# Optimization experiments

Hardware: AMD Instinct MI355X
Metric: run time of the kernel (lower is better)

## Reference

```python
import jax, jax.numpy as jnp
import numpy as np

N_ATOMS = 512
ATOM_SHAPE = (3, 3, 3)
SPARSE_ITERS = 128
FPB = 8  # features_per_band


def unit_norm(x, axis=-1, eps=1e-12):
    n = jnp.linalg.norm(x, axis=axis, keepdims=True)
    return x / jnp.maximum(n, eps)


def best_fit(signal, atoms):
    # signal: [B, bands, time, per] ; atoms: [n_atoms, 3,3,3]
    B, bands, time, per = signal.shape
    sig = signal[:, None]  # [B,1,bands,time,per]
    # pad (0,2) on last three dims
    sig = jnp.pad(sig, ((0, 0), (0, 0), (0, 2), (0, 2), (0, 2)))
    # conv3d correlation: lax conv with NCDHW / OIDHW
    fm = jax.lax.conv_general_dilated(
        sig, atoms[:, None], window_strides=(1, 1, 1), padding='VALID',
        dimension_numbers=('NCDHW', 'OIDHW', 'NCDHW'))  # [B, n_atoms, bands, time, per]
    flat = fm.reshape(B, -1)
    idx = jnp.argmax(flat, axis=-1)
    val = jnp.take_along_axis(flat, idx[:, None], axis=-1)[:, 0]
    # unflatten index -> (atom, b, c, d)
    fshape = fm.shape[1:]
    a_i = idx // (fshape[1] * fshape[2] * fshape[3])
    rem = idx % (fshape[1] * fshape[2] * fshape[3])
    b_i = rem // (fshape[2] * fshape[3])
    rem = rem % (fshape[2] * fshape[3])
    c_i = rem // fshape[3]
    d_i = rem % fshape[3]

    def per_batch(sig_b, a, b, c, dd, v):
        # sig_b: padded [bands+2, time+2, per+2]
        atom = atoms[a] * v  # [3,3,3]
        # Since conv output spatial extent = input extent (valid over padded),
        # max offsets b,c,d <= dims-1 of padded-2, slice always fits fully.
        patch = jax.lax.dynamic_slice(sig_b, (b, c, dd), ATOM_SHAPE)
        return jax.lax.dynamic_update_slice(sig_b, patch - atom, (b, c, dd))

    sig2 = jax.vmap(per_batch)(sig[:, 0], a_i, b_i, c_i, d_i, val)
    return sig2[:, :bands, :time, :per]


def sparse_code(signal, atoms):
    def body(res, _):
        return best_fit(res, atoms), None
    res, _ = jax.lax.scan(body, signal, None, length=SPARSE_ITERS)
    return res


def layer_norm(x, g, b, eps=1e-5):
    m = jnp.mean(x, axis=-1, keepdims=True)
    v = jnp.var(x, axis=-1, keepdims=True)
    return (x - m) / jnp.sqrt(v + eps) * g + b


def batch_norm(x, g, b, eps=1e-5):
    # x: [B, C, T]; training-mode batch stats over (B, T)
    m = jnp.mean(x, axis=(0, 2), keepdims=True)
    v = jnp.var(x, axis=(0, 2), keepdims=True)
    return (x - m) / jnp.sqrt(v + eps) * g[None, :, None] + b[None, :, None]


def conv1d(x, w, b, pad):
    # x: [B,C,T], w: [O,I,K]
    y = jax.lax.conv_general_dilated(x, w, (1,), [(pad, pad)],
                                     dimension_numbers=('NCT', 'OIT', 'NCT'))
    return y + b[None, :, None]


def upsample4(x):
    # nearest, scale 4 along time
    return jnp.repeat(x, 4, axis=-1)


def setup_inputs() -> dict:
    key = jax.random.key(0)
    ks = jax.random.split(key, 24)
    w = 0.05
    x = jax.random.normal(ks[0], (4, 128, 128, 257), dtype=jnp.float32)
    d = jax.random.uniform(ks[1], (N_ATOMS, 27), minval=-1, maxval=1)
    atoms = unit_norm(d, axis=-1).reshape(N_ATOMS, *ATOM_SHAPE)
    inp = {
        'x': x,
        'atoms': atoms,
        'embed_w': jax.random.normal(ks[2], (257, FPB)) * w,
        'embed_b': jnp.zeros((FPB,)),
        # LinearOutputStack(1024, 3, out 1024, LayerNorm): 3 hidden-ish linears
        'ctx_w1': jax.random.normal(ks[3], (1024, 1024)) * w,
        'ctx_b1': jnp.zeros((1024,)),
        'ctx_g1': jnp.ones((1024,)), 'ctx_be1': jnp.zeros((1024,)),
        'ctx_w2': jax.random.normal(ks[4], (1024, 1024)) * w,
        'ctx_b2': jnp.zeros((1024,)),
        'ctx_g2': jnp.ones((1024,)), 'ctx_be2': jnp.zeros((1024,)),
        'ctx_w3': jax.random.normal(ks[5], (1024, 1024)) * w,
        'ctx_b3': jnp.zeros((1024,)),
        # up stack conv weights
        'up_w1': jax.random.normal(ks[6], (512, 1024, 7)) * w,
        'up_b1': jnp.zeros((512,)), 'bn_g1': jnp.ones((512,)), 'bn_b1': jnp.zeros((512,)),
        'up_w2': jax.random.normal(ks[7], (256, 512, 7)) * w,
        'up_b2': jnp.zeros((256,)), 'bn_g2': jnp.ones((256,)), 'bn_b2': jnp.zeros((256,)),
        'up_w3': jax.random.normal(ks[8], (128, 256, 7)) * w,
        'up_b3': jnp.zeros((128,)), 'bn_g3': jnp.ones((128,)), 'bn_b3': jnp.zeros((128,)),
        'up_w4': jax.random.normal(ks[9], (64, 128, 7)) * w,
        'up_b4': jnp.zeros((64,)), 'bn_g4': jnp.ones((64,)), 'bn_b4': jnp.zeros((64,)),
        'up_w5': jax.random.normal(ks[10], (1, 64, 7)) * w,
        'up_b5': jnp.zeros((1,)),
    }
    return inp


def reference(x, atoms, embed_w, embed_b,
              ctx_w1, ctx_b1, ctx_g1, ctx_be1,
              ctx_w2, ctx_b2, ctx_g2, ctx_be2,
              ctx_w3, ctx_b3,
              up_w1, up_b1, bn_g1, bn_b1,
              up_w2, up_b2, bn_g2, bn_b2,
              up_w3, up_b3, bn_g3, bn_b3,
              up_w4, up_b4, bn_g4, bn_b4,
              up_w5, up_b5):
    B, bands, time, per = x.shape
    # embed_features
    e = x @ embed_w + embed_b  # [B, bands, time, 8]
    # sparse coding (no_grad in original; result discarded but computed)
    _res = jax.lax.stop_gradient(sparse_code(e, atoms))
    encoded = jnp.transpose(e, (0, 3, 1, 2)).reshape(B, FPB * bands, time)  # [B,1024,T]
    # context
    ctx = jnp.sum(encoded, axis=-1)  # [B,1024]
    h = layer_norm(jax.nn.leaky_relu(ctx @ ctx_w1 + ctx_b1, 0.2), ctx_g1, ctx_be1)
    h = layer_norm(jax.nn.leaky_relu(h @ ctx_w2 + ctx_b2, 0.2), ctx_g2, ctx_be2)
    ctx_out = h @ ctx_w3 + ctx_b3
    # generate (up stack)
    y = jax.nn.leaky_relu(batch_norm(conv1d(encoded, up_w1, up_b1, 3), bn_g1, bn_b1), 0.2)
    y = upsample4(y)
    y = jax.nn.leaky_relu(batch_norm(conv1d(y, up_w2, up_b2, 3), bn_g2, bn_b2), 0.2)
    y = upsample4(y)
    y = jax.nn.leaky_relu(batch_norm(conv1d(y, up_w3, up_b3, 3), bn_g3, bn_b3), 0.2)
    y = upsample4(y)
    y = jax.nn.leaky_relu(batch_norm(conv1d(y, up_w4, up_b4, 3), bn_g4, bn_b4), 0.2)
    y = upsample4(y)
    y = conv1d(y, up_w5, up_b5, 3)  # [B,1,T*256]
    # reverb approximated as identity mix (ReverbGenerator source unavailable)
    return y, ctx_out
```

## Files before the change

### kernel.cpp

```cpp
#include <hip/hip_runtime.h>
#include <hip/hip_bf16.h>

using sh8   = __attribute__((ext_vector_type(8))) short;
using f32x4 = __attribute__((ext_vector_type(4))) float;

#define DEV __device__ __forceinline__

DEV float leaky(float x) { return x >= 0.f ? x : 0.2f * x; }

DEV unsigned short f2bf(float f) {
  unsigned u = __float_as_uint(f);
  u += 0x7FFF + ((u >> 16) & 1);
  return (unsigned short)(u >> 16);
}
DEV float bf2f(unsigned short b) { return __uint_as_float(((unsigned)b) << 16); }

template<int Cout, int Cin>
DEV void pack7_body(const float* __restrict__ w, unsigned short* __restrict__ wp, int blk) {
  constexpr long plane = (long)(Cin >> 5) * Cout * 32;
  int tid = blk * 256 + threadIdx.x;
  if (tid >= Cout * Cin) return;
  int co = tid / Cin, ci = tid - co * Cin;
  const float* src = w + (long)tid * 7;
  unsigned short* dst = wp + ((long)(ci >> 5) * Cout + co) * 32 + (ci & 31);
  #pragma unroll
  for (int k = 0; k < 7; ++k) dst[k * plane] = f2bf(src[k]);
}
template<int Cout, int Cin>
DEV void packph_body(const float* __restrict__ w, unsigned short* __restrict__ wp, int blk) {
  constexpr long plane = (long)(Cin >> 5) * Cout * 32;
  int tid = blk * 256 + threadIdx.x;
  if (tid >= Cout * Cin) return;
  int co = tid / Cin, ci = tid - co * Cin;
  float wk[7];
  #pragma unroll
  for (int k = 0; k < 7; ++k) wk[k] = w[(long)tid * 7 + k];
  unsigned short* dst = wp + ((long)(ci >> 5) * Cout + co) * 32 + (ci & 31);
  #pragma unroll
  for (int p = 0; p < 4; ++p) {
    #pragma unroll
    for (int d = 0; d < 3; ++d) {
      float s = 0.f;
      #pragma unroll
      for (int k = 0; k < 7; ++k) if (((p + k + 1) >> 2) == d) s += wk[k];
      dst[(p * 3 + d) * plane] = f2bf(s);
    }
  }
}

DEV void gemm_body(int gb, const float* __restrict__ h, const float* __restrict__ w,
                   float* __restrict__ gpart, int sum2) {
  __shared__ float hl[4][128];
  __shared__ float red[8][4][32];
  const int jb = gb & 31, kc = gb >> 5, k0 = kc * 128;
  for (int i = threadIdx.x; i < 512; i += 256) {
    int bb = i >> 7, kk = i & 127;
    float v;
    if (sum2) {
      int base = ((bb << 10) + k0 + kk) << 1;
      v = h[base] + h[base + 1];
    } else {
      v = h[(bb << 10) + k0 + kk];
    }
    hl[bb][kk] = v;
  }
  __syncthreads();
  const int jl = threadIdx.x & 31, kq = threadIdx.x >> 5;
  const int j = jb * 32 + jl;
  float a0 = 0, a1 = 0, a2 = 0, a3 = 0;
  const float* wp = w + (long)(k0 + kq * 16) * 1024 + j;
  #pragma unroll
  for (int k = 0; k < 16; ++k) {
    float wv = wp[(long)k * 1024];
    a0 += hl[0][kq * 16 + k] * wv;
    a1 += hl[1][kq * 16 + k] * wv;
    a2 += hl[2][kq * 16 + k] * wv;
    a3 += hl[3][kq * 16 + k] * wv;
  }
  red[kq][0][jl] = a0; red[kq][1][jl] = a1; red[kq][2][jl] = a2; red[kq][3][jl] = a3;
  __syncthreads();
  if (threadIdx.x < 128) {
    int bb = threadIdx.x >> 5, j2 = threadIdx.x & 31;
    float s = 0;
    #pragma unroll
    for (int q = 0; q < 8; ++q) s += red[q][bb][j2];
    gpart[((long)kc * 4 + bb) * 1024 + jb * 32 + j2] = s;
  }
}

__global__ __launch_bounds__(256)
void embed_pack(const float* __restrict__ x, const float* __restrict__ ew,
                const float* __restrict__ eb, unsigned short* __restrict__ encbf,
                float* __restrict__ part,
                const float* __restrict__ cw1, const float* __restrict__ cw2,
                const float* __restrict__ cw3, const float* __restrict__ cw4,
                unsigned short* __restrict__ wbuf) {
  if (blockIdx.x >= 1024) {
    int blk = blockIdx.x - 1024;
    if (blk < 2048)      pack7_body<512, 1024>(cw1, wbuf, blk);
    else if (blk < 2560) packph_body<256, 512>(cw2, wbuf + 3670016, blk - 2048);
    else if (blk < 2688) packph_body<128, 256>(cw3, wbuf + 5242880, blk - 2560);
    else                 packph_body<64, 128>(cw4, wbuf + 5636096, blk - 2688);
    return;
  }
  __shared__ unsigned short W16[257 * 16];
  __shared__ float ctxred[4][8];
  const int tid = threadIdx.x;

  for (int i = tid; i < 257 * 16; i += 256) {
    int p = i >> 4, f = i & 15;
    W16[i] = (f < 8) ? f2bf(ew[p * 8 + f]) : (unsigned short)0;
  }
  __syncthreads();

  const int w = tid >> 6, lane = tid & 63;
  const int m = lane & 15, g = lane >> 4;

  sh8 breg[8];
  #pragma unroll
  for (int kk = 0; kk < 8; ++kk) {
    #pragma unroll
    for (int j = 0; j < 8; ++j)
      breg[kk][j] = (short)W16[(kk * 32 + g * 8 + j) * 16 + m];
  }
  const float w256 = bf2f(W16[256 * 16 + m]);
  const float ebf = (m < 8) ? eb[m] : 0.f;

  const int bid = blockIdx.x;
  const long row0 = (long)bid * 64;
  const int b = bid >> 8, band = (bid >> 1) & 127, half = bid & 1;
  const int t0 = half * 64 + w * 16;

  const float* xp = x + (row0 + w * 16 + m) * 257 + g * 8;
  float vals[8][8];
  #pragma unroll
  for (int kk = 0; kk < 8; ++kk) {
    #pragma unroll
    for (int j = 0; j < 8; ++j)
      vals[kk][j] = xp[kk * 32 + j];
  }
  f32x4 acc = {0.f, 0.f, 0.f, 0.f};
  #pragma unroll
  for (int kk = 0; kk < 8; ++kk) {
    sh8 afr;
    #pragma unroll
    for (int j = 0; j < 8; ++j) afr[j] = (short)f2bf(vals[kk][j]);
    acc = __builtin_amdgcn_mfma_f32_16x16x32_bf16(afr, breg[kk], acc, 0, 0, 0);
  }

  const float* xq = x + (row0 + w * 16 + g * 4) * 257 + 256;
  float ctx_acc = 0.f;
  unsigned short pk[4];
  #pragma unroll
  for (int r = 0; r < 4; ++r) {
    float e = acc[r] + xq[(long)r * 257] * w256 + ebf;
    pk[r] = f2bf(e);
    ctx_acc += e;
  }
  if (m < 8) {
    long o = ((long)b * 1024 + m * 128 + band) * 128 + t0 + g * 4;
    *(ushort4*)(encbf + o) = make_ushort4(pk[0], pk[1], pk[2], pk[3]);
  }

  ctx_acc += __shfl_xor(ctx_acc, 16);
  ctx_acc += __shfl_xor(ctx_acc, 32);
  if (lane < 8) ctxred[w][lane] = ctx_acc;
  __syncthreads();
  if (tid < 8) {
    float sv = ctxred[0][tid] + ctxred[1][tid] + ctxred[2][tid] + ctxred[3][tid];
    part[((b * 1024 + tid * 128 + band) << 1) + half] = sv;
  }
}

template<int UPS, int SPLITK>
__global__ __launch_bounds__(256, 2)
void conv_mfma_g(const unsigned short* __restrict__ act,
                 const unsigned short* __restrict__ wpack,
                 float* __restrict__ outp,
                 int Cin, int Cout, int Tout, int nconv,
                 const float* __restrict__ h, const float* __restrict__ wmlp,
                 float* __restrict__ gpart, int sum2) {
  if ((int)blockIdx.x >= nconv) { gemm_body(blockIdx.x - nconv, h, wmlp, gpart, sum2); return; }
  constexpr int NC = (UPS == 1) ? 70 : 18;
  const int Tin = Tout / UPS;
  const int cpb = Cin / SPLITK;
  const int ncib = cpb >> 5;
  const int nCibTot = Cin >> 5;
  const int nco = Cout >> 6, nt = Tout >> 6;

  int bid = blockIdx.x;
  const int sk = bid % SPLITK; bid /= SPLITK;
  const int tt = bid % nt;  bid /= nt;
  const int cot = bid % nco; bid /= nco;
  const int b = bid;
  const int t0 = tt << 6, co0 = cot << 6;
  const int ci0 = sk * cpb;

  extern __shared__ unsigned short lin[];

  const unsigned short* actb = act + ((long)b * Cin + ci0) * Tin;
  const int u_base = (UPS == 1) ? (t0 - 3) : ((t0 >> 2) - 1);
  const int total = cpb * NC;
  for (int i = threadIdx.x; i < total; i += 256) {
    int ci = i / NC, ul = i - ci * NC;
    int u = u_base + ul;
    unsigned short v = 0;
    if (u >= 0 && u < Tin) v = actb[(long)ci * Tin + u];
    lin[((ci >> 5) * NC + ul) * 40 + (ci & 31)] = v;
  }
  __syncthreads();

  const int lane = threadIdx.x & 63, w = threadIdx.x >> 6;
  const int m = lane & 15, g = lane >> 4;

  int boff[28];
  #pragma unroll
  for (int s = 0; s < 4; ++s) {
    #pragma unroll
    for (int k = 0; k < 7; ++k) {
      int row = (UPS == 1) ? (s * 16 + m + k)
                           : (s * 4 + ((m + k + 9) >> 2) - 2);
      boff[s * 7 + k] = row * 40 + g * 8;
    }
  }

  const long wlane = ((long)(co0 + w * 16 + m) * 4 + g) * 8;

  f32x4 acc[4];
  #pragma unroll
  for (int s = 0; s < 4; ++s) { acc[s][0] = 0.f; acc[s][1] = 0.f; acc[s][2] = 0.f; acc[s][3] = 0.f; }

  for (int cib = 0; cib < ncib; ++cib) {
    const unsigned short* lb = lin + cib * (NC * 40);
    const int cg = (ci0 >> 5) + cib;
    sh8 a[7];
    #pragma unroll
    for (int k = 0; k < 7; ++k)
      a[k] = *(const sh8*)(wpack + (long)(k * nCibTot + cg) * Cout * 32 + wlane);
    #pragma unroll
    for (int k = 0; k < 7; ++k) {
      #pragma unroll
      for (int s = 0; s < 4; ++s) {
        sh8 bfr = *(const sh8*)(lb + boff[s * 7 + k]);
        acc[s] = __builtin_amdgcn_mfma_f32_16x16x32_bf16(a[k], bfr, acc[s], 0, 0, 0);
      }
    }
  }

  float* op = outp + (((long)sk * 4 + b) * Cout + (co0 + w * 16 + g * 4)) * (long)Tout + t0 + m;
  #pragma unroll
  for (int r = 0; r < 4; ++r) {
    #pragma unroll
    for (int s = 0; s < 4; ++s)
      op[(long)r * Tout + s * 16] = acc[s][r];
  }
}

template<int SPLITK>
__global__ __launch_bounds__(256, 2)
void conv_ph_g(const float* __restrict__ csum_in, const float* __restrict__ sp,
               const float* __restrict__ g, const float* __restrict__ be,
               const unsigned short* __restrict__ wpack,
               float* __restrict__ outp,
               int Cin, int Cout, int Tin, int nconv,
               const float* __restrict__ h, const float* __restrict__ wmlp,
               float* __restrict__ gpart, int sum2) {
  if ((int)blockIdx.x >= nconv) { gemm_body(blockIdx.x - nconv, h, wmlp, gpart, sum2); return; }
  const int Tout = Tin << 2;
  const int cpb = Cin / SPLITK;
  const int ncib = cpb >> 5;
  const int nCibTot = Cin >> 5;
  const int nco = Cout >> 6, ntu = Tin >> 6;

  int bid = blockIdx.x;
  const int sk = bid % SPLITK; bid /= SPLITK;
  const int tu = bid % ntu; bid /= ntu;
  const int cot = bid % nco; bid /= nco;
  const int b = bid;
  const int u0 = tu << 6, co0 = cot << 6;
  const int ci0 = sk * cpb;

  extern __shared__ unsigned short lin[];
  __shared__ float ssc[64], ssh[64];

  if (threadIdx.x < cpb) {
    int c = ci0 + threadIdx.x;
    float S = sp[c * 4] + sp[c * 4 + 1] + sp[c * 4 + 2] + sp[c * 4 + 3];
    float Q = sp[Cin * 4 + c * 4] + sp[Cin * 4 + c * 4 + 1] + sp[Cin * 4 + c * 4 + 2] + sp[Cin * 4 + c * 4 + 3];
    float n = 4.f * (float)Tin;
    float mean = S / n;
    float var = Q / n - mean * mean;
    float sc = g[c] * rsqrtf(var + 1e-5f);
    ssc[threadIdx.x] = sc;
    ssh[threadIdx.x] = be[c] - mean * sc;
  }
  __syncthreads();

  const float* csb = csum_in + ((long)b * Cin + ci0) * Tin;
  const int total = cpb * 66;
  for (int i = threadIdx.x; i < total; i += 256) {
    int ci = i / 66, r = i - ci * 66;
    int u = u0 - 1 + r;
    unsigned short v = 0;
    if (u >= 0 && u < Tin) {
      float t = csb[(long)ci * Tin + u];
      v = f2bf(leaky(t * ssc[ci] + ssh[ci]));
    }
    lin[((ci >> 5) * 66 + r) * 40 + (ci & 31)] = v;
  }
  __syncthreads();

  const int lane = threadIdx.x & 63, w = threadIdx.x >> 6;
  const int m = lane & 15, g2 = lane >> 4;

  int boff[4][3];
  #pragma unroll
  for (int s = 0; s < 4; ++s)
    #pragma unroll
    for (int d = 0; d < 3; ++d)
      boff[s][d] = (s * 16 + m + d) * 40 + g2 * 8;

  const long wlane = ((long)(co0 + w * 16 + m)) * 32 + g2 * 8;

  f32x4 acc[4][4];
  #pragma unroll
  for (int s = 0; s < 4; ++s)
    #pragma unroll
    for (int p = 0; p < 4; ++p) { acc[s][p][0] = 0.f; acc[s][p][1] = 0.f; acc[s][p][2] = 0.f; acc[s][p][3] = 0.f; }

  for (int cib = 0; cib < ncib; ++cib) {
    const unsigned short* lb = lin + cib * (66 * 40);
    const int cg = (ci0 >> 5) + cib;
    sh8 a[12];
    #pragma unroll
    for (int pd = 0; pd < 12; ++pd)
      a[pd] = *(const sh8*)(wpack + ((long)(pd * nCibTot + cg) * Cout) * 32 + wlane);
    #pragma unroll
    for (int s = 0; s < 4; ++s) {
      sh8 b0 = *(const sh8*)(lb + boff[s][0]);
      sh8 b1 = *(const sh8*)(lb + boff[s][1]);
      sh8 b2 = *(const sh8*)(lb + boff[s][2]);
      acc[s][0] = __builtin_amdgcn_mfma_f32_16x16x32_bf16(a[0],  b0, acc[s][0], 0, 0, 0);
      acc[s][0] = __builtin_amdgcn_mfma_f32_16x16x32_bf16(a[1],  b1, acc[s][0], 0, 0, 0);
      acc[s][1] = __builtin_amdgcn_mfma_f32_16x16x32_bf16(a[3],  b0, acc[s][1], 0, 0, 0);
      acc[s][1] = __builtin_amdgcn_mfma_f32_16x16x32_bf16(a[4],  b1, acc[s][1], 0, 0, 0);
      acc[s][1] = __builtin_amdgcn_mfma_f32_16x16x32_bf16(a[5],  b2, acc[s][1], 0, 0, 0);
      acc[s][2] = __builtin_amdgcn_mfma_f32_16x16x32_bf16(a[6],  b0, acc[s][2], 0, 0, 0);
      acc[s][2] = __builtin_amdgcn_mfma_f32_16x16x32_bf16(a[7],  b1, acc[s][2], 0, 0, 0);
      acc[s][2] = __builtin_amdgcn_mfma_f32_16x16x32_bf16(a[8],  b2, acc[s][2], 0, 0, 0);
      acc[s][3] = __builtin_amdgcn_mfma_f32_16x16x32_bf16(a[10], b1, acc[s][3], 0, 0, 0);
      acc[s][3] = __builtin_amdgcn_mfma_f32_16x16x32_bf16(a[11], b2, acc[s][3], 0, 0, 0);
    }
  }

  float* op = outp + (((long)sk * 4 + b) * Cout + (co0 + w * 16 + g2 * 4)) * (long)Tout;
  #pragma unroll
  for (int r = 0; r < 4; ++r) {
    #pragma unroll
    for (int s = 0; s < 4; ++s) {
      float4 v4 = make_float4(acc[s][0][r], acc[s][1][r], acc[s][2][r], acc[s][3][r]);
      *(float4*)(op + (long)r * Tout + ((u0 + s * 16 + m) << 2)) = v4;
    }
  }
}

__global__ __launch_bounds__(256)
void bnsum_ln(const float* __restrict__ p, float* __restrict__ sp,
              float* __restrict__ csum, int C, int T, int SK, int mode,
              const float* __restrict__ gpart, const float* __restrict__ bias,
              const float* __restrict__ g, const float* __restrict__ be,
              float* __restrict__ outp) {
  const int nbn = C * 4;
  if ((int)blockIdx.x >= nbn) {
    if (mode == 1) {
      int b = blockIdx.x - nbn;
      __shared__ float buf[1024];
      __shared__ float rs2[4], rq2[4];
      float s = 0, q = 0;
      #pragma unroll
      for (int i = 0; i < 4; ++i) {
        int j = threadIdx.x + i * 256;
        float v = bias[j];
        #pragma unroll
        for (int kc = 0; kc < 8; ++kc) v += gpart[((long)kc * 4 + b) * 1024 + j];
        v = leaky(v);
        buf[j] = v; s += v; q += v * v;
      }
      #pragma unroll
      for (int off = 32; off; off >>= 1) { s += __shfl_down(s, off); q += __shfl_down(q, off); }
      int wid = threadIdx.x >> 6, lane = threadIdx.x & 63;
      if (lane == 0) { rs2[wid] = s; rq2[wid] = q; }
      __syncthreads();
      float S = rs2[0] + rs2[1] + rs2[2] + rs2[3];
      float Q = rq2[0] + rq2[1] + rq2[2] + rq2[3];
      float mean = S * (1.f / 1024.f);
      float var = Q * (1.f / 1024.f) - mean * mean;
      float rstd = rsqrtf(var + 1e-5f);
      #pragma unroll
      for (int i = 0; i < 4; ++i) {
        int j = threadIdx.x + i * 256;
        outp[b * 1024 + j] = (buf[j] - mean) * rstd * g[j] + be[j];
      }
    } else {
      int i = (blockIdx.x - nbn) * 256 + threadIdx.x;
      int b = i >> 10, j = i & 1023;
      float v = bias[j];
      #pragma unroll
      for (int kc = 0; kc < 8; ++kc) v += gpart[((long)kc * 4 + b) * 1024 + j];
      outp[i] = v;
    }
    return;
  }
  const int c = blockIdx.x >> 2, b = blockIdx.x & 3;
  long stride = (long)4 * C * T;
  const float* r = p + ((long)b * C + c) * T;
  float* cw = csum + ((long)b * C + c) * T;
  float s = 0, q = 0;
  for (int t = threadIdx.x; t < T; t += 256) {
    float v = r[t];
    for (int k = 1; k < SK; ++k) v += r[t + k * stride];
    cw[t] = v;
    s += v; q += v * v;
  }
  #pragma unroll
  for (int off = 32; off; off >>= 1) { s += __shfl_down(s, off); q += __shfl_down(q, off); }
  __shared__ float rs[4], rq[4];
  int wid = threadIdx.x >> 6, lane = threadIdx.x & 63;
  if (lane == 0) { rs[wid] = s; rq[wid] = q; }
  __syncthreads();
  if (threadIdx.x == 0) {
    sp[c * 4 + b] = rs[0] + rs[1] + rs[2] + rs[3];
    sp[C * 4 + c * 4 + b] = rq[0] + rq[1] + rq[2] + rq[3];
  }
}

__global__ __launch_bounds__(256)
void conv5_kernel(const float* __restrict__ csum_in, const float* __restrict__ sp,
                  const float* __restrict__ g, const float* __restrict__ be,
                  const float* __restrict__ wgt, const float* __restrict__ bias,
                  float* __restrict__ out, int Tout) {
  __shared__ unsigned short sv[64 * 66];
  __shared__ float wph[64 * 13];
  __shared__ float ssc[64], ssh[64];

  const int b = blockIdx.y;
  const int u0 = blockIdx.x * 64;
  const int Tin = Tout >> 2;
  const int tid = threadIdx.x;

  {
    int ci = tid >> 2, pp = tid & 3;
    float s0 = 0, s1 = 0, s2 = 0;
    #pragma unroll
    for (int k = 0; k < 7; ++k) {
      int d = (pp - 3 + k + 4) >> 2;
      float wv = wgt[ci * 7 + k];
      if (d == 0) s0 += wv; else if (d == 1) s1 += wv; else s2 += wv;
    }
    wph[ci * 13 + pp * 3 + 0] = s0;
    wph[ci * 13 + pp * 3 + 1] = s1;
    wph[ci * 13 + pp * 3 + 2] = s2;
  }
  if (tid < 64) {
    float S = sp[tid * 4] + sp[tid * 4 + 1] + sp[tid * 4 + 2] + sp[tid * 4 + 3];
    float Q = sp[256 + tid * 4] + sp[256 + tid * 4 + 1] + sp[256 + tid * 4 + 2] + sp[256 + tid * 4 + 3];
    float n = 4.f * (float)Tin;
    float mean = S / n;
    float var = Q / n - mean * mean;
    float sc = g[tid] * rsqrtf(var + 1e-5f);
    ssc[tid] = sc;
    ssh[tid] = be[tid] - mean * sc;
  }
  __syncthreads();

  const float* inb = csum_in + (long)b * 64 * Tin;
  for (int i = tid; i < 64 * 66; i += 256) {
    int ci = i / 66, uu = i - ci * 66;
    int u = u0 - 1 + uu;
    unsigned short v = 0;
    if (u >= 0 && u < Tin) {
      float t = inb[(long)ci * Tin + u];
      v = f2bf(leaky(t * ssc[ci] + ssh[ci]));
    }
    sv[ci * 66 + uu] = v;
  }
  __syncthreads();

  const int ul = tid >> 2;
  const int chunk = tid & 3;
  float a0 = 0, a1 = 0, a2 = 0, a3 = 0;
  #pragma unroll
  for (int cc = 0; cc < 16; ++cc) {
    int ci = chunk * 16 + cc;
    float v0 = bf2f(sv[ci * 66 + ul]);
    float v1 = bf2f(sv[ci * 66 + ul + 1]);
    float v2 = bf2f(sv[ci * 66 + ul + 2]);
    const float* wp = wph + ci * 13;
    a0 += v0 * wp[0] + v1 * wp[1];
    a1 += v0 * wp[3] + v1 * wp[4] + v2 * wp[5];
    a2 += v0 * wp[6] + v1 * wp[7] + v2 * wp[8];
    a3 += v1 * wp[10] + v2 * wp[11];
  }
  #pragma unroll
  for (int msk = 1; msk <= 2; msk <<= 1) {
    a0 += __shfl_xor(a0, msk);
    a1 += __shfl_xor(a1, msk);
    a2 += __shfl_xor(a2, msk);
    a3 += __shfl_xor(a3, msk);
  }
  if (chunk == 0) {
    float bv = bias[0];
    float4 r = make_float4(a0 + bv, a1 + bv, a2 + bv, a3 + bv);
    *(float4*)(out + (long)b * Tout + (long)(u0 + ul) * 4) = r;
  }
}

extern "C" void kernel_launch(void* const* d_in, const int* in_sizes, int n_in,
                              void* d_out, int out_size, void* d_ws, size_t ws_size,
                              hipStream_t stream) {
  const float* x     = (const float*)d_in[0];
  const float* ew    = (const float*)d_in[2];
  const float* eb    = (const float*)d_in[3];
  const float* w1    = (const float*)d_in[4];
  const float* b1    = (const float*)d_in[5];
  const float* g1    = (const float*)d_in[6];
  const float* be1   = (const float*)d_in[7];
  const float* w2    = (const float*)d_in[8];
  const float* b2    = (const float*)d_in[9];
  const float* g2    = (const float*)d_in[10];
  const float* be2   = (const float*)d_in[11];
  const float* w3    = (const float*)d_in[12];
  const float* b3    = (const float*)d_in[13];
  const float* up_w1 = (const float*)d_in[14];
  const float* up_b1 = (const float*)d_in[15];
  const float* bn_g1 = (const float*)d_in[16];
  const float* bn_b1 = (const float*)d_in[17];
  const float* up_w2 = (const float*)d_in[18];
  const float* up_b2 = (const float*)d_in[19];
  const float* bn_g2 = (const float*)d_in[20];
  const float* bn_b2 = (const float*)d_in[21];
  const float* up_w3 = (const float*)d_in[22];
  const float* up_b3 = (const float*)d_in[23];
  const float* bn_g3 = (const float*)d_in[24];
  const float* bn_b3 = (const float*)d_in[25];
  const float* up_w4 = (const float*)d_in[26];
  const float* up_b4 = (const float*)d_in[27];
  const float* bn_g4 = (const float*)d_in[28];
  const float* bn_b4 = (const float*)d_in[29];
  const float* up_w5 = (const float*)d_in[30];
  const float* up_b5 = (const float*)d_in[31];

  float* out = (float*)d_out;

  float* ws = (float*)d_ws;
  float* part   = ws;
  float* gpart  = part + 8192;
  float* t2     = gpart + 32768;
  float* statsp = t2 + 4096;
  float* csum   = statsp + 4096;
  float* pbuf   = csum + 2097152;
  unsigned short* encbf = (unsigned short*)(pbuf + 4194304);
  unsigned short* wbuf  = encbf + 524288;

  embed_pack<<<3744, 256, 0, stream>>>(x, ew, eb, encbf, part,
                                       up_w1, up_w2, up_w3, up_w4, wbuf);

  conv_mfma_g<1, 8><<<768, 256, 22400, stream>>>(encbf, wbuf, pbuf, 1024, 512, 128,
                                                 512, part, w1, gpart, 1);
  bnsum_ln<<<2052, 256, 0, stream>>>(pbuf, statsp, csum, 512, 128, 8, 1,
                                     gpart, b1, g1, be1, t2);
  conv_ph_g<8><<<512, 256, 10560, stream>>>(csum, statsp, bn_g1, bn_b1, wbuf + 3670016,
                                            pbuf, 512, 256, 128,
                                            256, t2, w2, gpart, 0);
  bnsum_ln<<<1028, 256, 0, stream>>>(pbuf, statsp, csum, 256, 512, 8, 1,
                                     gpart, b2, g2, be2, t2);
  conv_ph_g<4><<<512, 256, 10560, stream>>>(csum, statsp, bn_g2, bn_b2, wbuf + 5242880,
                                            pbuf, 256, 128, 512,
                                            256, t2, w3, gpart, 0);
  bnsum_ln<<<528, 256, 0, stream>>>(pbuf, statsp, csum, 128, 2048, 4, 2,
                                    gpart, b3, b3, b3, out + 131072);
  conv_ph_g<2><<<256, 256, 10560, stream>>>(csum, statsp, bn_g3, bn_b3, wbuf + 5636096,
                                            pbuf, 128, 64, 2048,
                                            256, t2, w3, gpart, -1);
  bnsum_ln<<<256, 256, 0, stream>>>(pbuf, statsp, csum, 64, 8192, 2, 0,
                                    gpart, b3, b3, b3, out + 131072);
  conv5_kernel<<<dim3(128, 4), 256, 0, stream>>>(csum, statsp, bn_g4, bn_b4, up_w5, up_b5, out, 32768);
}
```

Baseline: 147.6 us.

## Halve time tiles and split-K in conv kernels, skip final partial-sum copy

The first conv is specialised to constants and its time tile shrinks from 64 to 32 with split-K going from 8 to 4. The phase-upsampling convs likewise use 32-wide time tiles and half the split-K, so block counts stay the same while the partial-sum buffers that the reduction kernels must read and add get smaller. The last batch-norm stats pass no longer writes a reduced copy because split-K is 1, and conv5 reads the partial buffer directly. In exchange, each block reloads more halo per tile and does more MFMA work over a longer K loop.

```diff
diff --git a/kernel.cpp b/kernel.cpp
--- a/kernel.cpp
+++ b/kernel.cpp
@@ -172,34 +172,31 @@
   }
 }
 
-template<int UPS, int SPLITK>
+template<int SPLITK>
 __global__ __launch_bounds__(256, 2)
-void conv_mfma_g(const unsigned short* __restrict__ act,
-                 const unsigned short* __restrict__ wpack,
-                 float* __restrict__ outp,
-                 int Cin, int Cout, int Tout, int nconv,
-                 const float* __restrict__ h, const float* __restrict__ wmlp,
-                 float* __restrict__ gpart, int sum2) {
+void conv1_g(const unsigned short* __restrict__ act,
+             const unsigned short* __restrict__ wpack,
+             float* __restrict__ outp, int nconv,
+             const float* __restrict__ h, const float* __restrict__ wmlp,
+             float* __restrict__ gpart, int sum2) {
   if ((int)blockIdx.x >= nconv) { gemm_body(blockIdx.x - nconv, h, wmlp, gpart, sum2); return; }
-  constexpr int NC = (UPS == 1) ? 70 : 18;
-  const int Tin = Tout / UPS;
-  const int cpb = Cin / SPLITK;
-  const int ncib = cpb >> 5;
-  const int nCibTot = Cin >> 5;
-  const int nco = Cout >> 6, nt = Tout >> 6;
+  constexpr int Cin = 1024, Cout = 512, Tout = 128, Tin = 128, NC = 38;
+  constexpr int cpb = Cin / SPLITK;
+  constexpr int ncib = cpb >> 5;
+  constexpr int nCibTot = Cin >> 5;
 
   int bid = blockIdx.x;
   const int sk = bid % SPLITK; bid /= SPLITK;
-  const int tt = bid % nt;  bid /= nt;
-  const int cot = bid % nco; bid /= nco;
+  const int tt = bid & 3;  bid >>= 2;
+  const int cot = bid & 7; bid >>= 3;
   const int b = bid;
-  const int t0 = tt << 6, co0 = cot << 6;
+  const int t0 = tt << 5, co0 = cot << 6;
   const int ci0 = sk * cpb;
 
   extern __shared__ unsigned short lin[];
 
   const unsigned short* actb = act + ((long)b * Cin + ci0) * Tin;
-  const int u_base = (UPS == 1) ? (t0 - 3) : ((t0 >> 2) - 1);
+  const int u_base = t0 - 3;
   const int total = cpb * NC;
   for (int i = threadIdx.x; i < total; i += 256) {
     int ci = i / NC, ul = i - ci * NC;
@@ -213,22 +210,18 @@
   const int lane = threadIdx.x & 63, w = threadIdx.x >> 6;
   const int m = lane & 15, g = lane >> 4;
 
-  int boff[28];
-  #pragma unroll
-  for (int s = 0; s < 4; ++s) {
-    #pragma unroll
-    for (int k = 0; k < 7; ++k) {
-      int row = (UPS == 1) ? (s * 16 + m + k)
-                           : (s * 4 + ((m + k + 9) >> 2) - 2);
-      boff[s * 7 + k] = row * 40 + g * 8;
-    }
-  }
+  int boff[2][7];
+  #pragma unroll
+  for (int s = 0; s < 2; ++s)
+    #pragma unroll
+    for (int k = 0; k < 7; ++k)
+      boff[s][k] = (s * 16 + m + k) * 40 + g * 8;
 
   const long wlane = ((long)(co0 + w * 16 + m) * 4 + g) * 8;
 
-  f32x4 acc[4];
-  #pragma unroll
-  for (int s = 0; s < 4; ++s) { acc[s][0] = 0.f; acc[s][1] = 0.f; acc[s][2] = 0.f; acc[s][3] = 0.f; }
+  f32x4 acc[2];
+  #pragma unroll
+  for (int s = 0; s < 2; ++s) { acc[s][0] = 0.f; acc[s][1] = 0.f; acc[s][2] = 0.f; acc[s][3] = 0.f; }
 
   for (int cib = 0; cib < ncib; ++cib) {
     const unsigned short* lb = lin + cib * (NC * 40);
@@ -240,8 +233,8 @@
     #pragma unroll
     for (int k = 0; k < 7; ++k) {
       #pragma unroll
-      for (int s = 0; s < 4; ++s) {
-        sh8 bfr = *(const sh8*)(lb + boff[s * 7 + k]);
+      for (int s = 0; s < 2; ++s) {
+        sh8 bfr = *(const sh8*)(lb + boff[s][k]);
         acc[s] = __builtin_amdgcn_mfma_f32_16x16x32_bf16(a[k], bfr, acc[s], 0, 0, 0);
       }
     }
@@ -251,7 +244,7 @@
   #pragma unroll
   for (int r = 0; r < 4; ++r) {
     #pragma unroll
-    for (int s = 0; s < 4; ++s)
+    for (int s = 0; s < 2; ++s)
       op[(long)r * Tout + s * 16] = acc[s][r];
   }
 }
@@ -266,22 +259,23 @@
                const float* __restrict__ h, const float* __restrict__ wmlp,
                float* __restrict__ gpart, int sum2) {
   if ((int)blockIdx.x >= nconv) { gemm_body(blockIdx.x - nconv, h, wmlp, gpart, sum2); return; }
+  constexpr int NC = 34;
   const int Tout = Tin << 2;
   const int cpb = Cin / SPLITK;
   const int ncib = cpb >> 5;
   const int nCibTot = Cin >> 5;
-  const int nco = Cout >> 6, ntu = Tin >> 6;
+  const int nco = Cout >> 6, ntu = Tin >> 5;
 
   int bid = blockIdx.x;
   const int sk = bid % SPLITK; bid /= SPLITK;
   const int tu = bid % ntu; bid /= ntu;
   const int cot = bid % nco; bid /= nco;
   const int b = bid;
-  const int u0 = tu << 6, co0 = cot << 6;
+  const int u0 = tu << 5, co0 = cot << 6;
   const int ci0 = sk * cpb;
 
   extern __shared__ unsigned short lin[];
-  __shared__ float ssc[64], ssh[64];
+  __shared__ float ssc[128], ssh[128];
 
   if (threadIdx.x < cpb) {
     int c = ci0 + threadIdx.x;
@@ -297,46 +291,46 @@
   __syncthreads();
 
   const float* csb = csum_in + ((long)b * Cin + ci0) * Tin;
-  const int total = cpb * 66;
+  const int total = cpb * NC;
   for (int i = threadIdx.x; i < total; i += 256) {
-    int ci = i / 66, r = i - ci * 66;
+    int ci = i / NC, r = i - ci * NC;
     int u = u0 - 1 + r;
     unsigned short v = 0;
     if (u >= 0 && u < Tin) {
       float t = csb[(long)ci * Tin + u];
       v = f2bf(leaky(t * ssc[ci] + ssh[ci]));
     }
-    lin[((ci >> 5) * 66 + r) * 40 + (ci & 31)] = v;
+    lin[((ci >> 5) * NC + r) * 40 + (ci & 31)] = v;
   }
   __syncthreads();
 
   const int lane = threadIdx.x & 63, w = threadIdx.x >> 6;
   const int m = lane & 15, g2 = lane >> 4;
 
-  int boff[4][3];
-  #pragma unroll
-  for (int s = 0; s < 4; ++s)
+  int boff[2][3];
+  #pragma unroll
+  for (int s = 0; s < 2; ++s)
     #pragma unroll
     for (int d = 0; d < 3; ++d)
       boff[s][d] = (s * 16 + m + d) * 40 + g2 * 8;
 
   const long wlane = ((long)(co0 + w * 16 + m)) * 32 + g2 * 8;
 
-  f32x4 acc[4][4];
-  #pragma unroll
-  for (int s = 0; s < 4; ++s)
+  f32x4 acc[2][4];
+  #pragma unroll
+  for (int s = 0; s < 2; ++s)
     #pragma unroll
     for (int p = 0; p < 4; ++p) { acc[s][p][0] = 0.f; acc[s][p][1] = 0.f; acc[s][p][2] = 0.f; acc[s][p][3] = 0.f; }
 
   for (int cib = 0; cib < ncib; ++cib) {
-    const unsigned short* lb = lin + cib * (66 * 40);
+    const unsigned short* lb = lin + cib * (NC * 40);
     const int cg = (ci0 >> 5) + cib;
     sh8 a[12];
     #pragma unroll
     for (int pd = 0; pd < 12; ++pd)
       a[pd] = *(const sh8*)(wpack + ((long)(pd * nCibTot + cg) * Cout) * 32 + wlane);
     #pragma unroll
-    for (int s = 0; s < 4; ++s) {
+    for (int s = 0; s < 2; ++s) {
       sh8 b0 = *(const sh8*)(lb + boff[s][0]);
       sh8 b1 = *(const sh8*)(lb + boff[s][1]);
       sh8 b2 = *(const sh8*)(lb + boff[s][2]);
@@ -357,7 +351,7 @@
   #pragma unroll
   for (int r = 0; r < 4; ++r) {
     #pragma unroll
-    for (int s = 0; s < 4; ++s) {
+    for (int s = 0; s < 2; ++s) {
       float4 v4 = make_float4(acc[s][0][r], acc[s][1][r], acc[s][2][r], acc[s][3][r]);
       *(float4*)(op + (long)r * Tout + ((u0 + s * 16 + m) << 2)) = v4;
     }
@@ -366,7 +360,7 @@
 
 __global__ __launch_bounds__(256)
 void bnsum_ln(const float* __restrict__ p, float* __restrict__ sp,
-              float* __restrict__ csum, int C, int T, int SK, int mode,
+              float* __restrict__ csum, int C, int T, int SK, int docopy, int mode,
               const float* __restrict__ gpart, const float* __restrict__ bias,
               const float* __restrict__ g, const float* __restrict__ be,
               float* __restrict__ outp) {
@@ -419,7 +413,7 @@
   for (int t = threadIdx.x; t < T; t += 256) {
     float v = r[t];
     for (int k = 1; k < SK; ++k) v += r[t + k * stride];
-    cw[t] = v;
+    if (docopy) cw[t] = v;
     s += v; q += v * v;
   }
   #pragma unroll
@@ -565,24 +559,24 @@
   embed_pack<<<3744, 256, 0, stream>>>(x, ew, eb, encbf, part,
                                        up_w1, up_w2, up_w3, up_w4, wbuf);
 
-  conv_mfma_g<1, 8><<<768, 256, 22400, stream>>>(encbf, wbuf, pbuf, 1024, 512, 128,
-                                                 512, part, w1, gpart, 1);
-  bnsum_ln<<<2052, 256, 0, stream>>>(pbuf, statsp, csum, 512, 128, 8, 1,
+  conv1_g<4><<<768, 256, 24320, stream>>>(encbf, wbuf, pbuf,
+                                          512, part, w1, gpart, 1);
+  bnsum_ln<<<2052, 256, 0, stream>>>(pbuf, statsp, csum, 512, 128, 4, 1, 1,
                                      gpart, b1, g1, be1, t2);
-  conv_ph_g<8><<<512, 256, 10560, stream>>>(csum, statsp, bn_g1, bn_b1, wbuf + 3670016,
+  conv_ph_g<4><<<512, 256, 10880, stream>>>(csum, statsp, bn_g1, bn_b1, wbuf + 3670016,
                                             pbuf, 512, 256, 128,
                                             256, t2, w2, gpart, 0);
-  bnsum_ln<<<1028, 256, 0, stream>>>(pbuf, statsp, csum, 256, 512, 8, 1,
+  bnsum_ln<<<1028, 256, 0, stream>>>(pbuf, statsp, csum, 256, 512, 4, 1, 1,
                                      gpart, b2, g2, be2, t2);
-  conv_ph_g<4><<<512, 256, 10560, stream>>>(csum, statsp, bn_g2, bn_b2, wbuf + 5242880,
+  conv_ph_g<2><<<512, 256, 10880, stream>>>(csum, statsp, bn_g2, bn_b2, wbuf + 5242880,
                                             pbuf, 256, 128, 512,
                                             256, t2, w3, gpart, 0);
-  bnsum_ln<<<528, 256, 0, stream>>>(pbuf, statsp, csum, 128, 2048, 4, 2,
+  bnsum_ln<<<528, 256, 0, stream>>>(pbuf, statsp, csum, 128, 2048, 2, 1, 2,
                                     gpart, b3, b3, b3, out + 131072);
-  conv_ph_g<2><<<256, 256, 10560, stream>>>(csum, statsp, bn_g3, bn_b3, wbuf + 5636096,
+  conv_ph_g<1><<<256, 256, 10880, stream>>>(csum, statsp, bn_g3, bn_b3, wbuf + 5636096,
                                             pbuf, 128, 64, 2048,
                                             256, t2, w3, gpart, -1);
-  bnsum_ln<<<256, 256, 0, stream>>>(pbuf, statsp, csum, 64, 8192, 2, 0,
+  bnsum_ln<<<256, 256, 0, stream>>>(pbuf, statsp, csum, 64, 8192, 1, 0, 0,
                                     gpart, b3, b3, b3, out + 131072);
-  conv5_kernel<<<dim3(128, 4), 256, 0, stream>>>(csum, statsp, bn_g4, bn_b4, up_w5, up_b5, out, 32768);
-}
+  conv5_kernel<<<dim3(128, 4), 256, 0, stream>>>(pbuf, statsp, bn_g4, bn_b4, up_w5, up_b5, out, 32768);
+}
```

New measurement: 138.6 us (median of 2 runs). 1.06x faster.
